# Kernel optimization log

Hardware: AMD Instinct MI355X
Metric: run time of the kernel (lower is better)

The kernel has to match this reference:

```python
import jax, jax.numpy as jnp
import numpy as np


def _flip_neg(a):
    # index k -> a[(-k) mod n] along last axis (torch.roll(torch.flip(a,-1),1,-1))
    return jnp.roll(jnp.flip(a, axis=-1), 1, axis=-1)


def setup_inputs() -> dict:
    key = jax.random.key(0)
    k1, k2 = jax.random.split(key)
    B, C, L, M = 16, 64, 65536, 512
    x = jax.random.normal(k1, (B, C, L), dtype=jnp.float32)
    scale = 1.0 / (C * C)
    weights1 = scale * jax.random.uniform(k2, (C, C, M), dtype=jnp.float32)
    return {"x": x, "weights1": weights1}


def reference(x, weights1):
    B, Cin, L = x.shape
    M = weights1.shape[-1]
    two_pi = jnp.asarray(2.0 * np.pi, dtype=x.dtype)

    # pseudo-DHT: elementwise modulation along length
    k = jnp.arange(L, dtype=x.dtype)
    theta = two_pi * k / L
    x_ht = x * (jnp.cos(theta) - jnp.sin(theta))  # (B, Cin, L)

    # mode-limited channel mixing (compl_mul1d)
    x1 = x_ht[:, :, :M]                 # (B, Cin, M)
    x1n = _flip_neg(x1)
    wn = _flip_neg(weights1)
    out_m = 0.5 * (
        jnp.einsum('bix,iox->box', x1, weights1)
        - jnp.einsum('bix,iox->box', x1n, wn)
        + jnp.einsum('bix,iox->box', x1, wn)
        + jnp.einsum('bix,iox->box', x1n, weights1)
    )  # (B, Cout, M)

    # zero-init half-spectrum buffer, slice-assign low modes
    Lh = L // 2 + 1
    Cout = weights1.shape[1]
    out = jnp.zeros((B, Cout, Lh), dtype=x.dtype).at[:, :, :M].set(out_m)

    # idht: same pseudo-DHT on the (B, Cout, Lh) buffer, normalized by size(1)=channels
    k2 = jnp.arange(Lh, dtype=x.dtype)
    theta2 = two_pi * k2 / Lh
    out = out * (jnp.cos(theta2) - jnp.sin(theta2)) / Cin
    return out
```

## Files before the change

### kernel.cpp

```cpp
#include <hip/hip_runtime.h>
#include <math.h>

#define B_   16
#define CIN  64
#define COUT 64
#define L_   65536
#define M_   512
#define LH_  32769

#define NBLK     2048
#define NTHREADS (NBLK * 256)
#define N4       ((B_ * COUT * LH_) / 4)

__global__ __launch_bounds__(256) void fused_spectral(
    const float* __restrict__ x, const float* __restrict__ w, float* __restrict__ out)
{
    const int tid = blockIdx.x * 256 + threadIdx.x;

    for (int j = tid; j < N4; j += NTHREADS) {
        const unsigned flat = (unsigned)j * 4u;
        const unsigned row  = flat / (unsigned)LH_;
        const unsigned col  = flat - row * (unsigned)LH_;
        if (col >= (unsigned)M_ && col <= (unsigned)(LH_ - 4)) {
            const float4 z = {0.f, 0.f, 0.f, 0.f};
            reinterpret_cast<float4*>(out)[j] = z;
        } else {
            #pragma unroll
            for (int e = 0; e < 4; ++e) {
                const unsigned f  = flat + (unsigned)e;
                const unsigned r2 = f / (unsigned)LH_;
                const unsigned c2_ = f - r2 * (unsigned)LH_;
                if (c2_ >= (unsigned)M_) out[f] = 0.f;
            }
        }
    }

    if (threadIdx.x >= 64) return;
    const int ctid = blockIdx.x * 64 + (int)threadIdx.x;
    const int m  = ctid & (M_ - 1);
    const int og = (ctid >> 9) & 15;
    const int b  = ctid >> 13;
    const int o0 = og * 4;
    const int m2 = (M_ - m) & (M_ - 1);

    const float TWO_PI = 6.28318530717958647692f;
    const float t1  = TWO_PI * (float)m  / (float)L_;
    const float t1n = TWO_PI * (float)m2 / (float)L_;
    const float t2  = TWO_PI * (float)m  / (float)LH_;
    const float c1m = cosf(t1)  - sinf(t1);
    const float c1n = cosf(t1n) - sinf(t1n);
    const float c2  = (cosf(t2) - sinf(t2)) * (1.0f / (float)CIN);

    float acc[4] = {0.f, 0.f, 0.f, 0.f};
    const float* xb = x + (size_t)b * CIN * L_;
    for (int i = 0; i < CIN; ++i) {
        const float xm = xb[(size_t)i * L_ + m]  * c1m;
        const float xn = xb[(size_t)i * L_ + m2] * c1n;
        const float* wr = w + ((size_t)i * COUT + o0) * M_;
        #pragma unroll
        for (int oo = 0; oo < 4; ++oo) {
            const float wm = wr[(size_t)oo * M_ + m];
            const float wn = wr[(size_t)oo * M_ + m2];
            acc[oo] += xm * (wm + wn) + xn * (wm - wn);
        }
    }

    #pragma unroll
    for (int oo = 0; oo < 4; ++oo)
        out[(size_t)(b * COUT + o0 + oo) * LH_ + m] = 0.5f * c2 * acc[oo];
}

extern "C" void kernel_launch(void* const* d_in, const int* in_sizes, int n_in,
                              void* d_out, int out_size, void* d_ws, size_t ws_size,
                              hipStream_t stream) {
    const float* x = (const float*)d_in[0];
    const float* w = (const float*)d_in[1];
    float* out = (float*)d_out;

    fused_spectral<<<NBLK, 256, 0, stream>>>(x, w, out);
}
```

Measured before the change: 38.55 us.

## Compute four modes by two outputs per thread with vectorized mirrored loads

Each compute thread now handles four consecutive modes for two output channels instead of one mode for four channels. It loads x and weights as float4 for both the forward and the mirrored (negative-frequency) index, reversing lanes in registers. Only even blocks run the compute phase, so the number of compute threads matches the new per-thread work. The goal is fewer scalar gather loads and better coalescing. The cost is that half as many blocks carry the compute tail, and the unaligned float4 loads may split into smaller accesses.

Result: slower. 90.22 us (+134.0%).

```diff
diff --git a/kernel.cpp b/kernel.cpp
--- a/kernel.cpp
+++ b/kernel.cpp
@@ -11,6 +11,13 @@
 #define NBLK     2048
 #define NTHREADS (NBLK * 256)
 #define N4       ((B_ * COUT * LH_) / 4)
+
+__device__ __forceinline__ float4 ld4u(const float* p) {
+    float4 v; __builtin_memcpy(&v, p, sizeof(float4)); return v;
+}
+__device__ __forceinline__ void st4u(float* p, float4 v) {
+    __builtin_memcpy(p, &v, sizeof(float4));
+}
 
 __global__ __launch_bounds__(256) void fused_spectral(
     const float* __restrict__ x, const float* __restrict__ w, float* __restrict__ out)
@@ -35,39 +42,71 @@
         }
     }
 
-    if (threadIdx.x >= 64) return;
-    const int ctid = blockIdx.x * 64 + (int)threadIdx.x;
-    const int m  = ctid & (M_ - 1);
-    const int og = (ctid >> 9) & 15;
-    const int b  = ctid >> 13;
-    const int o0 = og * 4;
-    const int m2 = (M_ - m) & (M_ - 1);
+    if ((blockIdx.x & 1) || threadIdx.x >= 64) return;
+    const int ctid = (int)(blockIdx.x >> 1) * 64 + (int)threadIdx.x;
+    const int mg = ctid & 127;
+    const int op = (ctid >> 7) & 31;
+    const int b  = ctid >> 12;
+    const int m0 = mg * 4;
+    const int o0 = op * 2;
+    const int roff = mg ? (509 - m0) : 508;
 
     const float TWO_PI = 6.28318530717958647692f;
-    const float t1  = TWO_PI * (float)m  / (float)L_;
-    const float t1n = TWO_PI * (float)m2 / (float)L_;
-    const float t2  = TWO_PI * (float)m  / (float)LH_;
-    const float c1m = cosf(t1)  - sinf(t1);
-    const float c1n = cosf(t1n) - sinf(t1n);
-    const float c2  = (cosf(t2) - sinf(t2)) * (1.0f / (float)CIN);
+    float c1m[4], c1n[4], c2v[4];
+    #pragma unroll
+    for (int e = 0; e < 4; ++e) {
+        const int m  = m0 + e;
+        const int m2 = (M_ - m) & (M_ - 1);
+        const float t1  = TWO_PI * (float)m  / (float)L_;
+        const float t1n = TWO_PI * (float)m2 / (float)L_;
+        const float t2  = TWO_PI * (float)m  / (float)LH_;
+        c1m[e] = cosf(t1)  - sinf(t1);
+        c1n[e] = cosf(t1n) - sinf(t1n);
+        c2v[e] = (cosf(t2) - sinf(t2)) * (0.5f / (float)CIN);
+    }
 
-    float acc[4] = {0.f, 0.f, 0.f, 0.f};
+    float acc0[4] = {0.f,0.f,0.f,0.f};
+    float acc1[4] = {0.f,0.f,0.f,0.f};
     const float* xb = x + (size_t)b * CIN * L_;
+
     for (int i = 0; i < CIN; ++i) {
-        const float xm = xb[(size_t)i * L_ + m]  * c1m;
-        const float xn = xb[(size_t)i * L_ + m2] * c1n;
-        const float* wr = w + ((size_t)i * COUT + o0) * M_;
+        const float* xr = xb + (size_t)i * L_;
+        const float4 xf = ld4u(xr + m0);
+        const float4 xl = ld4u(xr + roff);
+        float xm[4], xn[4];
+        xm[0] = xf.x * c1m[0]; xm[1] = xf.y * c1m[1];
+        xm[2] = xf.z * c1m[2]; xm[3] = xf.w * c1m[3];
+        float r0, r1, r2, r3;
+        if (mg) { r0 = xl.w; r1 = xl.z; r2 = xl.y; r3 = xl.x; }
+        else    { r0 = xr[0]; r1 = xl.w; r2 = xl.z; r3 = xl.y; }
+        xn[0] = r0 * c1n[0]; xn[1] = r1 * c1n[1];
+        xn[2] = r2 * c1n[2]; xn[3] = r3 * c1n[3];
+
+        const float* wi = w + (size_t)(i * COUT + o0) * M_;
         #pragma unroll
-        for (int oo = 0; oo < 4; ++oo) {
-            const float wm = wr[(size_t)oo * M_ + m];
-            const float wn = wr[(size_t)oo * M_ + m2];
-            acc[oo] += xm * (wm + wn) + xn * (wm - wn);
+        for (int oo = 0; oo < 2; ++oo) {
+            const float* wr = wi + (size_t)oo * M_;
+            const float4 wf = ld4u(wr + m0);
+            const float4 wl = ld4u(wr + roff);
+            float n0, n1, n2, n3;
+            if (mg) { n0 = wl.w; n1 = wl.z; n2 = wl.y; n3 = wl.x; }
+            else    { n0 = wr[0]; n1 = wl.w; n2 = wl.z; n3 = wl.y; }
+            float* acc = oo ? acc1 : acc0;
+            acc[0] += xm[0] * (wf.x + n0) + xn[0] * (wf.x - n0);
+            acc[1] += xm[1] * (wf.y + n1) + xn[1] * (wf.y - n1);
+            acc[2] += xm[2] * (wf.z + n2) + xn[2] * (wf.z - n2);
+            acc[3] += xm[3] * (wf.w + n3) + xn[3] * (wf.w - n3);
         }
     }
 
     #pragma unroll
-    for (int oo = 0; oo < 4; ++oo)
-        out[(size_t)(b * COUT + o0 + oo) * LH_ + m] = 0.5f * c2 * acc[oo];
+    for (int oo = 0; oo < 2; ++oo) {
+        float* acc = oo ? acc1 : acc0;
+        float4 r;
+        r.x = acc[0] * c2v[0]; r.y = acc[1] * c2v[1];
+        r.z = acc[2] * c2v[2]; r.w = acc[3] * c2v[3];
+        st4u(out + (size_t)(b * COUT + o0 + oo) * LH_ + m0, r);
+    }
 }
 
 extern "C" void kernel_launch(void* const* d_in, const int* in_sizes, int n_in,
```

## Specialize waves into compute and zero-fill roles with 4x2 register tiling

Applied to the files above, without the earlier changes.

Rather than having every wave zero-fill and then run compute, each wave is assigned one role: one in eight waves computes the channel mixing, and the rest fill the zero region. Compute waves now tile 4 batches by 2 output channels per thread, so each weight pair is reused across batches. This lets compute overlap the bandwidth-bound fill instead of running after it. The cost is more registers and fewer threads on compute, plus a possible load imbalance between the two roles.

Result: slower. 70.89 us (+83.9%).

```diff
diff --git a/kernel.cpp b/kernel.cpp
--- a/kernel.cpp
+++ b/kernel.cpp
@@ -8,16 +8,78 @@
 #define M_   512
 #define LH_  32769
 
-#define NBLK     2048
-#define NTHREADS (NBLK * 256)
-#define N4       ((B_ * COUT * LH_) / 4)
+#define NBLK       2048
+#define N4         ((B_ * COUT * LH_) / 4)
+#define NWAVES     (NBLK * 4)
+#define NCOMPWAVES 1024
+#define NFILLTHREADS ((NWAVES - NCOMPWAVES) * 64)
 
 __global__ __launch_bounds__(256) void fused_spectral(
     const float* __restrict__ x, const float* __restrict__ w, float* __restrict__ out)
 {
-    const int tid = blockIdx.x * 256 + threadIdx.x;
+    const int wv   = (int)threadIdx.x >> 6;
+    const int lane = (int)threadIdx.x & 63;
+    const int gw   = (int)blockIdx.x * 4 + wv;
 
-    for (int j = tid; j < N4; j += NTHREADS) {
+    if ((gw & 7) == 0) {
+        const int cw = gw >> 3;
+        const int m  = ((cw & 7) << 6) + lane;
+        const int o0 = ((cw >> 3) & 31) * 2;
+        const int b0 = (cw >> 8) * 4;
+        const int m2 = (M_ - m) & (M_ - 1);
+
+        const float TWO_PI = 6.28318530717958647692f;
+        const float t1  = TWO_PI * (float)m  / (float)L_;
+        const float t1n = TWO_PI * (float)m2 / (float)L_;
+        const float t2  = TWO_PI * (float)m  / (float)LH_;
+        const float c1m = cosf(t1)  - sinf(t1);
+        const float c1n = cosf(t1n) - sinf(t1n);
+        const float c2  = (cosf(t2) - sinf(t2)) * (0.5f / (float)CIN);
+
+        float acc[4][2];
+        #pragma unroll
+        for (int bb = 0; bb < 4; ++bb) { acc[bb][0] = 0.f; acc[bb][1] = 0.f; }
+
+        const float* xb0 = x + (size_t)(b0 + 0) * CIN * L_;
+        const float* xb1 = x + (size_t)(b0 + 1) * CIN * L_;
+        const float* xb2 = x + (size_t)(b0 + 2) * CIN * L_;
+        const float* xb3 = x + (size_t)(b0 + 3) * CIN * L_;
+
+        #pragma unroll 4
+        for (int i = 0; i < CIN; ++i) {
+            const size_t ro = (size_t)i * L_;
+            const float xm0 = xb0[ro + m] * c1m, xn0 = xb0[ro + m2] * c1n;
+            const float xm1 = xb1[ro + m] * c1m, xn1 = xb1[ro + m2] * c1n;
+            const float xm2v = xb2[ro + m] * c1m, xn2v = xb2[ro + m2] * c1n;
+            const float xm3 = xb3[ro + m] * c1m, xn3 = xb3[ro + m2] * c1n;
+
+            const float* wr = w + (size_t)(i * COUT + o0) * M_;
+            const float wm0 = wr[m],      wn0 = wr[m2];
+            const float wm1 = wr[M_ + m], wn1 = wr[M_ + m2];
+            const float ws0 = wm0 + wn0, wd0 = wm0 - wn0;
+            const float ws1 = wm1 + wn1, wd1 = wm1 - wn1;
+
+            acc[0][0] += xm0 * ws0 + xn0 * wd0;
+            acc[1][0] += xm1 * ws0 + xn1 * wd0;
+            acc[2][0] += xm2v * ws0 + xn2v * wd0;
+            acc[3][0] += xm3 * ws0 + xn3 * wd0;
+            acc[0][1] += xm0 * ws1 + xn0 * wd1;
+            acc[1][1] += xm1 * ws1 + xn1 * wd1;
+            acc[2][1] += xm2v * ws1 + xn2v * wd1;
+            acc[3][1] += xm3 * ws1 + xn3 * wd1;
+        }
+
+        #pragma unroll
+        for (int bb = 0; bb < 4; ++bb)
+            #pragma unroll
+            for (int oo = 0; oo < 2; ++oo)
+                out[(size_t)((b0 + bb) * COUT + o0 + oo) * LH_ + m] = c2 * acc[bb][oo];
+        return;
+    }
+
+    const int fwave = gw - ((gw + 7) >> 3);
+    const int ft = fwave * 64 + lane;
+    for (int j = ft; j < N4; j += NFILLTHREADS) {
         const unsigned flat = (unsigned)j * 4u;
         const unsigned row  = flat / (unsigned)LH_;
         const unsigned col  = flat - row * (unsigned)LH_;
@@ -34,40 +96,6 @@
             }
         }
     }
-
-    if (threadIdx.x >= 64) return;
-    const int ctid = blockIdx.x * 64 + (int)threadIdx.x;
-    const int m  = ctid & (M_ - 1);
-    const int og = (ctid >> 9) & 15;
-    const int b  = ctid >> 13;
-    const int o0 = og * 4;
-    const int m2 = (M_ - m) & (M_ - 1);
-
-    const float TWO_PI = 6.28318530717958647692f;
-    const float t1  = TWO_PI * (float)m  / (float)L_;
-    const float t1n = TWO_PI * (float)m2 / (float)L_;
-    const float t2  = TWO_PI * (float)m  / (float)LH_;
-    const float c1m = cosf(t1)  - sinf(t1);
-    const float c1n = cosf(t1n) - sinf(t1n);
-    const float c2  = (cosf(t2) - sinf(t2)) * (1.0f / (float)CIN);
-
-    float acc[4] = {0.f, 0.f, 0.f, 0.f};
-    const float* xb = x + (size_t)b * CIN * L_;
-    for (int i = 0; i < CIN; ++i) {
-        const float xm = xb[(size_t)i * L_ + m]  * c1m;
-        const float xn = xb[(size_t)i * L_ + m2] * c1n;
-        const float* wr = w + ((size_t)i * COUT + o0) * M_;
-        #pragma unroll
-        for (int oo = 0; oo < 4; ++oo) {
-            const float wm = wr[(size_t)oo * M_ + m];
-            const float wn = wr[(size_t)oo * M_ + m2];
-            acc[oo] += xm * (wm + wn) + xn * (wm - wn);
-        }
-    }
-
-    #pragma unroll
-    for (int oo = 0; oo < 4; ++oo)
-        out[(size_t)(b * COUT + o0 + oo) * LH_ + m] = 0.5f * c2 * acc[oo];
 }
 
 extern "C" void kernel_launch(void* const* d_in, const int* in_sizes, int n_in,
```

## Split compute and zero-fill into separate kernels with 2x2 batch-output register tiling

Applied to the files above, without the earlier changes.

The fused kernel is split into two launches. The first computes the low modes using all 256 threads per block, with each thread accumulating a 2-batch by 2-output tile so that both x and w loads are reused in registers. The second is a standalone zero-fill kernel. This removes the situation where only 64 of 256 threads did compute after the fill loop, at the cost of an extra launch and serialising the two stages.

Result: slower. 89.07 us (+131.0%).

```diff
diff --git a/kernel.cpp b/kernel.cpp
--- a/kernel.cpp
+++ b/kernel.cpp
@@ -8,16 +8,64 @@
 #define M_   512
 #define LH_  32769
 
-#define NBLK     2048
-#define NTHREADS (NBLK * 256)
-#define N4       ((B_ * COUT * LH_) / 4)
+#define FILL_NBLK  2048
+#define FILL_NTHR  (FILL_NBLK * 256)
+#define N4         ((B_ * COUT * LH_) / 4)
 
-__global__ __launch_bounds__(256) void fused_spectral(
+__global__ __launch_bounds__(256) void spectral_compute(
     const float* __restrict__ x, const float* __restrict__ w, float* __restrict__ out)
 {
-    const int tid = blockIdx.x * 256 + threadIdx.x;
+    const int ctid = (int)blockIdx.x * 256 + (int)threadIdx.x;
+    const int m  = ctid & 511;
+    const int op = (ctid >> 9) & 31;
+    const int bp = ctid >> 14;
+    const int o0 = op * 2;
+    const int b0 = bp * 2;
+    const int m2 = (M_ - m) & (M_ - 1);
 
-    for (int j = tid; j < N4; j += NTHREADS) {
+    const float TWO_PI = 6.28318530717958647692f;
+    const float t1  = TWO_PI * (float)m  / (float)L_;
+    const float t1n = TWO_PI * (float)m2 / (float)L_;
+    const float t2  = TWO_PI * (float)m  / (float)LH_;
+    const float c1m = cosf(t1)  - sinf(t1);
+    const float c1n = cosf(t1n) - sinf(t1n);
+    const float c2  = (cosf(t2) - sinf(t2)) * (0.5f / (float)CIN);
+
+    float a00 = 0.f, a01 = 0.f, a10 = 0.f, a11 = 0.f;
+
+    const float* x0 = x + (size_t)b0 * CIN * L_;
+    const float* x1 = x0 + (size_t)CIN * L_;
+
+    #pragma unroll 4
+    for (int i = 0; i < CIN; ++i) {
+        const size_t ro = (size_t)i * L_;
+        const float xm0 = x0[ro + m]  * c1m;
+        const float xn0 = x0[ro + m2] * c1n;
+        const float xm1 = x1[ro + m]  * c1m;
+        const float xn1 = x1[ro + m2] * c1n;
+
+        const float* wr = w + (size_t)(i * COUT + o0) * M_;
+        const float wmA = wr[m],       wnA = wr[m2];
+        const float wmB = wr[M_ + m],  wnB = wr[M_ + m2];
+        const float wsA = wmA + wnA, wdA = wmA - wnA;
+        const float wsB = wmB + wnB, wdB = wmB - wnB;
+
+        a00 += xm0 * wsA + xn0 * wdA;
+        a01 += xm0 * wsB + xn0 * wdB;
+        a10 += xm1 * wsA + xn1 * wdA;
+        a11 += xm1 * wsB + xn1 * wdB;
+    }
+
+    out[(size_t)((b0 + 0) * COUT + o0 + 0) * LH_ + m] = c2 * a00;
+    out[(size_t)((b0 + 0) * COUT + o0 + 1) * LH_ + m] = c2 * a01;
+    out[(size_t)((b0 + 1) * COUT + o0 + 0) * LH_ + m] = c2 * a10;
+    out[(size_t)((b0 + 1) * COUT + o0 + 1) * LH_ + m] = c2 * a11;
+}
+
+__global__ __launch_bounds__(256) void spectral_fill(float* __restrict__ out)
+{
+    const int tid = (int)blockIdx.x * 256 + (int)threadIdx.x;
+    for (int j = tid; j < N4; j += FILL_NTHR) {
         const unsigned flat = (unsigned)j * 4u;
         const unsigned row  = flat / (unsigned)LH_;
         const unsigned col  = flat - row * (unsigned)LH_;
@@ -34,40 +82,6 @@
             }
         }
     }
-
-    if (threadIdx.x >= 64) return;
-    const int ctid = blockIdx.x * 64 + (int)threadIdx.x;
-    const int m  = ctid & (M_ - 1);
-    const int og = (ctid >> 9) & 15;
-    const int b  = ctid >> 13;
-    const int o0 = og * 4;
-    const int m2 = (M_ - m) & (M_ - 1);
-
-    const float TWO_PI = 6.28318530717958647692f;
-    const float t1  = TWO_PI * (float)m  / (float)L_;
-    const float t1n = TWO_PI * (float)m2 / (float)L_;
-    const float t2  = TWO_PI * (float)m  / (float)LH_;
-    const float c1m = cosf(t1)  - sinf(t1);
-    const float c1n = cosf(t1n) - sinf(t1n);
-    const float c2  = (cosf(t2) - sinf(t2)) * (1.0f / (float)CIN);
-
-    float acc[4] = {0.f, 0.f, 0.f, 0.f};
-    const float* xb = x + (size_t)b * CIN * L_;
-    for (int i = 0; i < CIN; ++i) {
-        const float xm = xb[(size_t)i * L_ + m]  * c1m;
-        const float xn = xb[(size_t)i * L_ + m2] * c1n;
-        const float* wr = w + ((size_t)i * COUT + o0) * M_;
-        #pragma unroll
-        for (int oo = 0; oo < 4; ++oo) {
-            const float wm = wr[(size_t)oo * M_ + m];
-            const float wn = wr[(size_t)oo * M_ + m2];
-            acc[oo] += xm * (wm + wn) + xn * (wm - wn);
-        }
-    }
-
-    #pragma unroll
-    for (int oo = 0; oo < 4; ++oo)
-        out[(size_t)(b * COUT + o0 + oo) * LH_ + m] = 0.5f * c2 * acc[oo];
 }
 
 extern "C" void kernel_launch(void* const* d_in, const int* in_sizes, int n_in,
@@ -77,5 +91,6 @@
     const float* w = (const float*)d_in[1];
     float* out = (float*)d_out;
 
-    fused_spectral<<<NBLK, 256, 0, stream>>>(x, w, out);
+    spectral_compute<<<512, 256, 0, stream>>>(x, w, out);
+    spectral_fill<<<FILL_NBLK, 256, 0, stream>>>(out);
 }
```
